# Kernel optimization log

Hardware: AMD Instinct MI355X
Metric: run time of the kernel (lower is better)

The kernel has to match this reference:

```python
import jax, jax.numpy as jnp
import numpy as np

USERNUM = 100_000
ITEMNUM = 50_000
EMBED_DIM = 64
N_INTERACTIONS = 2_000_000
NUM_LAYERS = 3
BATCH = 4096


def setup_inputs() -> dict:
    rng = np.random.default_rng(0)
    # random bipartite interactions: users 1..USERNUM, items 1..ITEMNUM
    u = rng.integers(1, USERNUM + 1, N_INTERACTIONS)
    it = rng.integers(1, ITEMNUM + 1, N_INTERACTIONS)
    # node ids: user k -> k, item j -> USERNUM + j (matches build_graph)
    rows = np.concatenate([u, USERNUM + it]).astype(np.int32)
    cols = np.concatenate([USERNUM + it, u]).astype(np.int32)
    n_nodes = USERNUM + ITEMNUM + 1
    # symmetric normalization D^-1/2 A D^-1/2 (duplicate edges sum, as in scipy COO)
    deg = np.bincount(rows, minlength=n_nodes).astype(np.float32)
    d_inv_sqrt = np.where(deg > 0, deg ** -0.5, 0.0).astype(np.float32)
    vals = (d_inv_sqrt[rows] * d_inv_sqrt[cols]).astype(np.float32)

    key = jax.random.key(0)
    k1, k2, k3, k4, k5 = jax.random.split(key, 5)
    # xavier_normal init: std = sqrt(2 / (fan_in + fan_out))
    u_std = np.sqrt(2.0 / (USERNUM + 1 + EMBED_DIM)).astype(np.float32)
    i_std = np.sqrt(2.0 / (ITEMNUM + 1 + EMBED_DIM)).astype(np.float32)
    user_table = jax.random.normal(k1, (USERNUM + 1, EMBED_DIM), jnp.float32) * u_std
    item_table = jax.random.normal(k2, (ITEMNUM + 1, EMBED_DIM), jnp.float32) * i_std

    user_ids = jax.random.randint(k3, (BATCH,), 0, USERNUM + 1)
    pos_seqs = jax.random.randint(k4, (BATCH,), 1, ITEMNUM + 1)
    neg_seqs = jax.random.randint(k5, (BATCH,), 1, ITEMNUM + 1)

    return {
        "user_table": user_table,
        "item_table": item_table,
        "vals": jnp.asarray(vals),
        "rows": jnp.asarray(rows),
        "cols": jnp.asarray(cols),
        "user_ids": user_ids,
        "pos_seqs": pos_seqs,
        "neg_seqs": neg_seqs,
    }


def reference(user_table, item_table, vals, rows, cols, user_ids, pos_seqs, neg_seqs):
    usernum = user_table.shape[0] - 1
    itemnum = item_table.shape[0] - 1
    n_nodes = usernum + itemnum + 1

    # ego embeddings: users 0..usernum, items 1..itemnum (skip item padding row)
    x = jnp.concatenate([user_table, item_table[1:]], axis=0)  # [n_nodes, D]

    # LightGCN propagation: x_{l+1} = A_norm @ x_l (SpMM via gather + segment_sum),
    # layer combination = mean over layers 0..NUM_LAYERS
    acc = x
    for _ in range(NUM_LAYERS):
        msgs = vals[:, None] * x[cols]              # [nnz, D]
        x = jax.ops.segment_sum(msgs, rows, num_segments=n_nodes)
        acc = acc + x
    all_emb = acc / (NUM_LAYERS + 1)

    uidx = jnp.clip(user_ids, 0, usernum)
    pidx = usernum + jnp.clip(pos_seqs, 1, itemnum)  # item j lives at row usernum + j
    nidx = usernum + jnp.clip(neg_seqs, 1, itemnum)

    u_emb = all_emb[uidx]
    pos_logits = jnp.sum(u_emb * all_emb[pidx], axis=-1)
    neg_logits = jnp.sum(u_emb * all_emb[nidx], axis=-1)
    return pos_logits, neg_logits
```

## Files before the change

### kernel.cpp

```cpp
#include <hip/hip_runtime.h>
#include <hip/hip_fp16.h>
#include <cstdint>
#include <cstddef>


typedef __attribute__((ext_vector_type(8))) _Float16 half8;

#define NB_SHIFT 8
#define BCAP 16000
#define P1_SRC 4096
#define P1_DIM 512

__global__ __launch_bounds__(P1_DIM) void partition_kernel(
    const int* __restrict__ rows, const int* __restrict__ cols,
    int* __restrict__ bucket_cursor, int* __restrict__ tmp,
    int M , int nb) {
    __shared__ int            lhist[1024];
    __shared__ int            loff[1024];
    __shared__ int            ldelta[1024];
    __shared__ int            wsum[8];
    __shared__ int            stage[2 * P1_SRC];
    __shared__ unsigned short bstage[2 * P1_SRC];
    int t = threadIdx.x;
    int lane = t & 63, wv = t >> 6;
    int base     = blockIdx.x * P1_SRC;
    int cnt_here = min(P1_SRC, M - base);
    int full4    = cnt_here >> 2;
    int rem      = cnt_here & 3;
    for (int i = t; i < 1024; i += P1_DIM) lhist[i] = 0;
    __syncthreads();
    const int4* rows4 = (const int4*)(rows + base);
    const int4* cols4 = (const int4*)(cols + base);
    int4 uu[2], vv[2];
    int  rka[8], rkb[8];
#pragma unroll
    for (int k = 0; k < 2; ++k) {
        int i4 = t + k * P1_DIM;
        if (i4 < full4) {
            uu[k] = rows4[i4];
            vv[k] = cols4[i4];
            int u4[4] = {uu[k].x, uu[k].y, uu[k].z, uu[k].w};
            int v4[4] = {vv[k].x, vv[k].y, vv[k].z, vv[k].w};
#pragma unroll
            for (int e = 0; e < 4; ++e) {
                rka[4 * k + e] = atomicAdd(&lhist[u4[e] >> NB_SHIFT], 1);
                rkb[4 * k + e] = atomicAdd(&lhist[v4[e] >> NB_SHIFT], 1);
            }
        }
    }
    int ur = 0, vr = 0, rkra = 0, rkrb = 0;
    bool has_rem = (t < rem);
    if (has_rem) {
        ur = rows[base + 4 * full4 + t];
        vr = cols[base + 4 * full4 + t];
        rkra = atomicAdd(&lhist[ur >> NB_SHIFT], 1);
        rkrb = atomicAdd(&lhist[vr >> NB_SHIFT], 1);
    }
    __syncthreads();
    int v0 = lhist[2 * t], v1 = lhist[2 * t + 1];
    int ts = v0 + v1;
    int sc = ts;
#pragma unroll
    for (int off = 1; off < 64; off <<= 1) {
        int x = __shfl_up(sc, off);
        if (lane >= off) sc += x;
    }
    if (lane == 63) wsum[wv] = sc;
    __syncthreads();
    int prefix = 0;
#pragma unroll
    for (int k = 0; k < 8; ++k) {
        int s = wsum[k];
        prefix += (k < wv) ? s : 0;
    }
    int run = prefix + sc - ts;
    loff[2 * t]     = run;
    loff[2 * t + 1] = run + v0;
#pragma unroll
    for (int k = 0; k < 2; ++k) {
        int b  = 2 * t + k;
        int vvk = (k == 0) ? v0 : v1;
        if (b < nb && vvk > 0) {
            int old = atomicAdd(&bucket_cursor[b], vvk);
            ldelta[b] = b * BCAP + old - loff[b];
        }
    }
    __syncthreads();
#pragma unroll
    for (int k = 0; k < 2; ++k) {
        int i4 = t + k * P1_DIM;
        if (i4 < full4) {
            int u4[4] = {uu[k].x, uu[k].y, uu[k].z, uu[k].w};
            int v4[4] = {vv[k].x, vv[k].y, vv[k].z, vv[k].w};
#pragma unroll
            for (int e = 0; e < 4; ++e) {
                int ub = u4[e] >> NB_SHIFT;
                int s1 = loff[ub] + rka[4 * k + e];
                stage[s1]  = ((u4[e] & 255) << 18) | v4[e];
                bstage[s1] = (unsigned short)ub;
                int vb = v4[e] >> NB_SHIFT;
                int s2 = loff[vb] + rkb[4 * k + e];
                stage[s2]  = ((v4[e] & 255) << 18) | u4[e];
                bstage[s2] = (unsigned short)vb;
            }
        }
    }
    if (has_rem) {
        int ub = ur >> NB_SHIFT;
        int s1 = loff[ub] + rkra;
        stage[s1]  = ((ur & 255) << 18) | vr;
        bstage[s1] = (unsigned short)ub;
        int vb = vr >> NB_SHIFT;
        int s2 = loff[vb] + rkrb;
        stage[s2]  = ((vr & 255) << 18) | ur;
        bstage[s2] = (unsigned short)vb;
    }
    __syncthreads();
    int total = 2 * cnt_here;
    for (int s = t; s < total; s += P1_DIM) {
        tmp[s + ldelta[bstage[s]]] = stage[s];
    }
}

__global__ __launch_bounds__(512) void finalize_kernel(
    const int* __restrict__ tmp, const int* __restrict__ bcur,
    int* __restrict__ row_ptr, float* __restrict__ dis,
    float* __restrict__ dis2, float* __restrict__ invd,
    int* __restrict__ cv, int n_nodes, int nb, int nnz) {
    __shared__ int rcnt[256];
    __shared__ int ccur[256];
    __shared__ int wsum[4];
    __shared__ int red[512];
    int b = blockIdx.x;
    int t = threadIdx.x;
    int lane = t & 63, wv = t >> 6;
    int partial = 0;
    for (int i = t; i < b; i += 512) partial += bcur[i];
    red[t] = partial;
    __syncthreads();
    for (int off = 256; off > 0; off >>= 1) {
        if (t < off) red[t] += red[t + off];
        __syncthreads();
    }
    int dbeg  = red[0];
    int count = bcur[b];
    int src   = b * BCAP;
    if (t < 256) rcnt[t] = 0;
    __syncthreads();
    for (int i = t; i < count; i += 512) {
        atomicAdd(&rcnt[tmp[src + i] >> 18], 1);
    }
    __syncthreads();
    int v = 0, sc = 0;
    if (t < 256) {
        v  = rcnt[t];
        sc = v;
#pragma unroll
        for (int off = 1; off < 64; off <<= 1) {
            int x = __shfl_up(sc, off);
            if (lane >= off) sc += x;
        }
        if (lane == 63) wsum[wv] = sc;
    }
    __syncthreads();
    if (t < 256) {
        int prefix = 0;
#pragma unroll
        for (int k = 0; k < 4; ++k) {
            int s = wsum[k];
            prefix += (k < wv) ? s : 0;
        }
        int ex = prefix + sc - v;
        ccur[t] = dbeg + ex;
        int row = (b << NB_SHIFT) + t;
        if (row < n_nodes) {
            row_ptr[row] = dbeg + ex;
            double dv = (double)v;
            dis[row]  = (v > 0) ? (float)(1.0 / sqrt(dv)) : 0.0f;
            dis2[row] = (v > 0) ? (float)(1.0 / dv) : 0.0f;
            invd[row] = (v > 0) ? (float)sqrt(dv) : 0.0f;
        }
    }
    if (b == nb - 1 && t == 0) row_ptr[n_nodes] = nnz;
    __syncthreads();
    for (int i = t; i < count; i += 512) {
        int p  = tmp[src + i];
        int rk = atomicAdd(&ccur[p >> 18], 1);
        cv[rk] = p & 0x3FFFF;
    }
}

__global__ __launch_bounds__(256) void convert_y0_kernel(
    const float4* __restrict__ ut4, const float4* __restrict__ it4,
    const float* __restrict__ dis, half8* __restrict__ Yh0,
    int usernum, int n_nodes) {
    int idx = blockIdx.x * 256 + threadIdx.x;
    int row = idx >> 3;
    if (row >= n_nodes) return;
    int c = idx & 7;
    float d = dis[row];
    const float4* srcp = (row <= usernum)
        ? (ut4 + (size_t)row * 16 + 2 * c)
        : (it4 + (size_t)(row - usernum) * 16 + 2 * c);
    float4 a = srcp[0];
    float4 e = srcp[1];
    half8 o;
    o[0] = (_Float16)(d * a.x); o[1] = (_Float16)(d * a.y);
    o[2] = (_Float16)(d * a.z); o[3] = (_Float16)(d * a.w);
    o[4] = (_Float16)(d * e.x); o[5] = (_Float16)(d * e.y);
    o[6] = (_Float16)(d * e.z); o[7] = (_Float16)(d * e.w);
    Yh0[(size_t)row * 8 + c] = o;
}

__device__ inline float csr_row_sum_h(const _Float16* __restrict__ Yh,
                                      const int* __restrict__ cv,
                                      int beg, int end, int g, int l8,
                                      float one) {
    float acc[8] = {0.f, 0.f, 0.f, 0.f, 0.f, 0.f, 0.f, 0.f};
    const char* Yb = (const char*)Yh;
    const char* cb = (const char*)cv;
    unsigned lo = (unsigned)l8 * 16u;
    int j = beg + g;
    for (; j + 8 < end; j += 16) {
        unsigned c0 = (unsigned)*(const int*)(cb + ((unsigned)j << 2));
        unsigned c1 = (unsigned)*(const int*)(cb + ((unsigned)(j + 8) << 2));
        half8 x0 = *(const half8*)(Yb + (c0 << 7) + lo);
        half8 x1 = *(const half8*)(Yb + (c1 << 7) + lo);
        half8 tt = x0 + x1;
#pragma unroll
        for (int k = 0; k < 8; ++k) {
            acc[k] += one * (float)tt[k];
        }
    }
    if (j < end) {
        unsigned c0 = (unsigned)*(const int*)(cb + ((unsigned)j << 2));
        half8 x0 = *(const half8*)(Yb + (c0 << 7) + lo);
#pragma unroll
        for (int k = 0; k < 8; ++k) {
            acc[k] += one * (float)x0[k];
        }
    }
    bool gb0 = (g & 1) != 0;
    bool gb1 = (g & 2) != 0;
    bool gb2 = (g & 4) != 0;
    float s0 = gb0 ? acc[0] : acc[4];
    float s1 = gb0 ? acc[1] : acc[5];
    float s2 = gb0 ? acc[2] : acc[6];
    float s3 = gb0 ? acc[3] : acc[7];
    float a0 = (gb0 ? acc[4] : acc[0]) + __shfl_xor(s0, 8);
    float a1 = (gb0 ? acc[5] : acc[1]) + __shfl_xor(s1, 8);
    float a2 = (gb0 ? acc[6] : acc[2]) + __shfl_xor(s2, 8);
    float a3 = (gb0 ? acc[7] : acc[3]) + __shfl_xor(s3, 8);
    float t0 = gb1 ? a0 : a2;
    float t1 = gb1 ? a1 : a3;
    float b0 = (gb1 ? a2 : a0) + __shfl_xor(t0, 16);
    float b1 = (gb1 ? a3 : a1) + __shfl_xor(t1, 16);
    float u = gb2 ? b0 : b1;
    float fin = (gb2 ? b1 : b0) + __shfl_xor(u, 32);
    return fin;
}

__device__ inline int lane_dim(int g, int l8) {
    return l8 * 8 + ((g & 1) * 4 + (g & 2) + (g >> 2));
}

__global__ __launch_bounds__(256) void spmm_y_kernel(
    const _Float16* __restrict__ Yin, _Float16* __restrict__ Yout,
    const int* __restrict__ row_ptr, const int* __restrict__ cv,
    const float* __restrict__ dis2, float one, int n_nodes) {
    int wid  = (blockIdx.x * blockDim.x + threadIdx.x) >> 6;
    int lane = threadIdx.x & 63;
    int g = lane >> 3, sub = lane & 7;
    int row = wid * 8 + g;
    bool ok = row < n_nodes;
    int beg = 0, end = 0;
    if (ok) {
        beg = row_ptr[row];
        end = row_ptr[row + 1];
    }
    float d2 = ok ? dis2[row] : 0.0f;
    const char* Yb = (const char*)Yin;
    const char* cb = (const char*)cv;
    unsigned lo = (unsigned)sub * 16u;
    float acc[8] = {0.f, 0.f, 0.f, 0.f, 0.f, 0.f, 0.f, 0.f};
    int len = end - beg;
    int mx = len;
    mx = max(mx, __shfl_xor(mx, 8));
    mx = max(mx, __shfl_xor(mx, 16));
    mx = max(mx, __shfl_xor(mx, 32));
    int iters = (mx + 7) >> 3;
    int j = beg;
    size_t jb = ((size_t)(unsigned)j) << 2;
    int r0 = *(const int*)(cb + jb);
    int r1 = *(const int*)(cb + jb + 4u);
    int r2 = *(const int*)(cb + jb + 8u);
    int r3 = *(const int*)(cb + jb + 12u);
    int r4 = *(const int*)(cb + jb + 16u);
    int r5 = *(const int*)(cb + jb + 20u);
    int r6 = *(const int*)(cb + jb + 24u);
    int r7 = *(const int*)(cb + jb + 28u);
    for (int it = 0; it < iters; ++it) {
        unsigned c0 = (unsigned)((j     < end) ? r0 : 0);
        unsigned c1 = (unsigned)((j + 1 < end) ? r1 : 0);
        unsigned c2 = (unsigned)((j + 2 < end) ? r2 : 0);
        unsigned c3 = (unsigned)((j + 3 < end) ? r3 : 0);
        unsigned c4 = (unsigned)((j + 4 < end) ? r4 : 0);
        unsigned c5 = (unsigned)((j + 5 < end) ? r5 : 0);
        unsigned c6 = (unsigned)((j + 6 < end) ? r6 : 0);
        unsigned c7 = (unsigned)((j + 7 < end) ? r7 : 0);
        half8 x0 = *(const half8*)(Yb + ((size_t)c0 << 7) + lo);
        half8 x1 = *(const half8*)(Yb + ((size_t)c1 << 7) + lo);
        half8 x2 = *(const half8*)(Yb + ((size_t)c2 << 7) + lo);
        half8 x3 = *(const half8*)(Yb + ((size_t)c3 << 7) + lo);
        half8 x4 = *(const half8*)(Yb + ((size_t)c4 << 7) + lo);
        half8 x5 = *(const half8*)(Yb + ((size_t)c5 << 7) + lo);
        half8 x6 = *(const half8*)(Yb + ((size_t)c6 << 7) + lo);
        half8 x7 = *(const half8*)(Yb + ((size_t)c7 << 7) + lo);
        j += 8;
        jb = ((size_t)(unsigned)j) << 2;
        r0 = *(const int*)(cb + jb);
        r1 = *(const int*)(cb + jb + 4u);
        r2 = *(const int*)(cb + jb + 8u);
        r3 = *(const int*)(cb + jb + 12u);
        r4 = *(const int*)(cb + jb + 16u);
        r5 = *(const int*)(cb + jb + 20u);
        r6 = *(const int*)(cb + jb + 24u);
        r7 = *(const int*)(cb + jb + 28u);
        half8 sA = (x0 + x1) + (x2 + x3);
        half8 sB = (x4 + x5) + (x6 + x7);
        half8 tt = sA + sB;
#pragma unroll
        for (int k = 0; k < 8; ++k) {
            acc[k] += one * (float)tt[k];
        }
    }
    if (ok) {
        half8 o;
#pragma unroll
        for (int k = 0; k < 8; ++k) o[k] = (_Float16)(acc[k] * d2);
        *(half8*)((char*)Yout + ((size_t)row << 7) + lo) = o;
    }
}

__global__ __launch_bounds__(256) void gather_logits_kernel(
    const float* __restrict__ ut, const float* __restrict__ itb,
    const _Float16* __restrict__ Y1, const _Float16* __restrict__ Y2,
    const int* __restrict__ row_ptr, const int* __restrict__ cv,
    const float* __restrict__ dis, const float* __restrict__ invd,
    const int* __restrict__ user_ids, const int* __restrict__ pos_seqs,
    const int* __restrict__ neg_seqs, float* __restrict__ out,
    float one, int usernum, int itemnum, int batch) {
    int w    = (blockIdx.x * blockDim.x + threadIdx.x) >> 6;
    int lane = threadIdx.x & 63;
    if (w >= batch) return;
    int g = lane >> 3, l8 = lane & 7;
    int d = lane_dim(g, l8);
    int idxs[3];
    int u = min(max(user_ids[w], 0), usernum);
    idxs[0] = u;
    int p = min(max(pos_seqs[w], 1), itemnum);
    idxs[1] = usernum + p;
    int nn = min(max(neg_seqs[w], 1), itemnum);
    idxs[2] = usernum + nn;
    float vals[3];
#pragma unroll
    for (int q = 0; q < 3; ++q) {
        int idx = idxs[q];
        int beg = row_ptr[idx];
        int end = row_ptr[idx + 1];
        float dr = dis[idx];
        float iv = invd[idx];
        float fin = csr_row_sum_h(Y2, cv, beg, end, g, l8, one);
        const float* base0 = (q == 0) ? (ut + (size_t)u * 64)
                                      : (itb + (size_t)(idx - usernum) * 64);
        float x0v = base0[d];
        float y1v = (float)Y1[(size_t)idx * 64 + d];
        float y2v = (float)Y2[(size_t)idx * 64 + d];
        vals[q] = x0v + iv * (y1v + y2v) + fin * dr;
    }
    float dp = vals[0] * vals[1];
    float dn = vals[0] * vals[2];
#pragma unroll
    for (int off = 1; off < 64; off <<= 1) {
        dp += __shfl_xor(dp, off);
        dn += __shfl_xor(dn, off);
    }
    if (lane == 0) {
        out[w]         = dp * 0.0625f;
        out[batch + w] = dn * 0.0625f;
    }
}

extern "C" void kernel_launch(void* const* d_in, const int* in_sizes, int n_in,
                              void* d_out, int out_size, void* d_ws,
                              size_t ws_size, hipStream_t stream) {
    const float* user_table = (const float*)d_in[0];
    const float* item_table = (const float*)d_in[1];
    const int*   rows       = (const int*)d_in[3];
    const int*   cols       = (const int*)d_in[4];
    const int*   user_ids   = (const int*)d_in[5];
    const int*   pos_seqs   = (const int*)d_in[6];
    const int*   neg_seqs   = (const int*)d_in[7];
    float*       out        = (float*)d_out;

    const int D = 64;
    int usernum = in_sizes[0] / D - 1;
    int itemnum = in_sizes[1] / D - 1;
    int nnz     = in_sizes[2];
    int batch   = in_sizes[5];
    int n_nodes = usernum + itemnum + 1;
    int nb      = (n_nodes + (1 << NB_SHIFT) - 1) >> NB_SHIFT;
    int M       = nnz >> 1;

    char* w = (char*)d_ws;
    auto alloc = [&](size_t bytes) {
        char* p = w;
        w += (bytes + 255) & ~(size_t)255;
        return p;
    };
    _Float16* Yh0   = (_Float16*)alloc((size_t)n_nodes * D * 2);
    _Float16* Yh1   = (_Float16*)alloc((size_t)n_nodes * D * 2);
    _Float16* Yh2   = (_Float16*)alloc((size_t)n_nodes * D * 2);
    int*   cv       = (int*)alloc((size_t)nnz * 4 + 8192);
    int*   row_ptr  = (int*)alloc((size_t)(n_nodes + 1) * 4);
    float* dis      = (float*)alloc((size_t)n_nodes * 4);
    float* dis2     = (float*)alloc((size_t)n_nodes * 4);
    float* invd     = (float*)alloc((size_t)n_nodes * 4);
    int*   bcur     = (int*)alloc(4096);
    int*   tmp      = (int*)Yh1;

    hipMemsetAsync(bcur, 0, 4096, stream);
    int p1_tiles = (M + P1_SRC - 1) / P1_SRC;
    partition_kernel<<<p1_tiles, P1_DIM, 0, stream>>>(rows, cols, bcur, tmp,
                                                      M, nb);
    finalize_kernel<<<nb, 512, 0, stream>>>(tmp, bcur, row_ptr, dis, dis2,
                                            invd, cv, n_nodes, nb, nnz);
    int conv_blocks = (n_nodes * 8 + 255) / 256;
    convert_y0_kernel<<<conv_blocks, 256, 0, stream>>>(
        (const float4*)user_table, (const float4*)item_table, dis,
        (half8*)Yh0, usernum, n_nodes);

    const float one = 1.0f;
    int spmm_grid = (n_nodes + 31) / 32;
    spmm_y_kernel<<<spmm_grid, 256, 0, stream>>>(Yh0, Yh1, row_ptr, cv, dis2,
                                                 one, n_nodes);
    spmm_y_kernel<<<spmm_grid, 256, 0, stream>>>(Yh1, Yh2, row_ptr, cv, dis2,
                                                 one, n_nodes);

    gather_logits_kernel<<<(batch + 3) / 4, 256, 0, stream>>>(
        user_table, item_table, Yh1, Yh2, row_ptr, cv, dis, invd, user_ids,
        pos_seqs, neg_seqs, out, one, usernum, itemnum, batch);
}
```

Measured before the change: 292.4 us.

## Split fp16 embeddings into two 32-dim halves processed by separate grid slices

Stores each layer's fp16 embedding matrix as two column halves (dims 0-31 and 32-63), each 64 bytes per row. The SpMM kernel gains a second grid dimension that selects the half and maps 4 lanes per row, so each wave handles 16 rows. The intent is to shrink the working set of each gather pass so it stays resident in cache, improving hit rates for the random column gathers. The cost is reading the CSR indices twice, once per half, plus more blocks and a slightly more complex gather in the logits kernel.

```diff
diff --git a/kernel.cpp b/kernel.cpp
--- a/kernel.cpp
+++ b/kernel.cpp
@@ -192,8 +192,8 @@
 
 __global__ __launch_bounds__(256) void convert_y0_kernel(
     const float4* __restrict__ ut4, const float4* __restrict__ it4,
-    const float* __restrict__ dis, half8* __restrict__ Yh0,
-    int usernum, int n_nodes) {
+    const float* __restrict__ dis, _Float16* __restrict__ YA,
+    _Float16* __restrict__ YB, int usernum, int n_nodes) {
     int idx = blockIdx.x * 256 + threadIdx.x;
     int row = idx >> 3;
     if (row >= n_nodes) return;
@@ -209,23 +209,26 @@
     o[2] = (_Float16)(d * a.z); o[3] = (_Float16)(d * a.w);
     o[4] = (_Float16)(d * e.x); o[5] = (_Float16)(d * e.y);
     o[6] = (_Float16)(d * e.z); o[7] = (_Float16)(d * e.w);
-    Yh0[(size_t)row * 8 + c] = o;
-}
-
-__device__ inline float csr_row_sum_h(const _Float16* __restrict__ Yh,
-                                      const int* __restrict__ cv,
-                                      int beg, int end, int g, int l8,
-                                      float one) {
+    _Float16* dst = (c < 4) ? (YA + (size_t)row * 32 + c * 8)
+                            : (YB + (size_t)row * 32 + (c - 4) * 8);
+    *(half8*)dst = o;
+}
+
+__device__ inline float csr_row_sum_h2(const _Float16* __restrict__ YA,
+                                       const _Float16* __restrict__ YB,
+                                       const int* __restrict__ cv,
+                                       int beg, int end, int g, int l8,
+                                       float one) {
     float acc[8] = {0.f, 0.f, 0.f, 0.f, 0.f, 0.f, 0.f, 0.f};
-    const char* Yb = (const char*)Yh;
+    const char* Yb = (const char*)(l8 < 4 ? YA : YB);
     const char* cb = (const char*)cv;
-    unsigned lo = (unsigned)l8 * 16u;
+    unsigned lo = (unsigned)(l8 & 3) * 16u;
     int j = beg + g;
     for (; j + 8 < end; j += 16) {
         unsigned c0 = (unsigned)*(const int*)(cb + ((unsigned)j << 2));
         unsigned c1 = (unsigned)*(const int*)(cb + ((unsigned)(j + 8) << 2));
-        half8 x0 = *(const half8*)(Yb + (c0 << 7) + lo);
-        half8 x1 = *(const half8*)(Yb + (c1 << 7) + lo);
+        half8 x0 = *(const half8*)(Yb + ((size_t)c0 << 6) + lo);
+        half8 x1 = *(const half8*)(Yb + ((size_t)c1 << 6) + lo);
         half8 tt = x0 + x1;
 #pragma unroll
         for (int k = 0; k < 8; ++k) {
@@ -234,7 +237,7 @@
     }
     if (j < end) {
         unsigned c0 = (unsigned)*(const int*)(cb + ((unsigned)j << 2));
-        half8 x0 = *(const half8*)(Yb + (c0 << 7) + lo);
+        half8 x0 = *(const half8*)(Yb + ((size_t)c0 << 6) + lo);
 #pragma unroll
         for (int k = 0; k < 8; ++k) {
             acc[k] += one * (float)x0[k];
@@ -265,13 +268,14 @@
 }
 
 __global__ __launch_bounds__(256) void spmm_y_kernel(
-    const _Float16* __restrict__ Yin, _Float16* __restrict__ Yout,
+    const _Float16* __restrict__ YinA, const _Float16* __restrict__ YinB,
+    _Float16* __restrict__ YoutA, _Float16* __restrict__ YoutB,
     const int* __restrict__ row_ptr, const int* __restrict__ cv,
     const float* __restrict__ dis2, float one, int n_nodes) {
     int wid  = (blockIdx.x * blockDim.x + threadIdx.x) >> 6;
     int lane = threadIdx.x & 63;
-    int g = lane >> 3, sub = lane & 7;
-    int row = wid * 8 + g;
+    int g = lane >> 2, sub = lane & 3;
+    int row = wid * 16 + g;
     bool ok = row < n_nodes;
     int beg = 0, end = 0;
     if (ok) {
@@ -279,12 +283,14 @@
         end = row_ptr[row + 1];
     }
     float d2 = ok ? dis2[row] : 0.0f;
-    const char* Yb = (const char*)Yin;
+    const char* Yb = (const char*)(blockIdx.y ? YinB : YinA);
+    _Float16*   Yo = blockIdx.y ? YoutB : YoutA;
     const char* cb = (const char*)cv;
     unsigned lo = (unsigned)sub * 16u;
     float acc[8] = {0.f, 0.f, 0.f, 0.f, 0.f, 0.f, 0.f, 0.f};
     int len = end - beg;
     int mx = len;
+    mx = max(mx, __shfl_xor(mx, 4));
     mx = max(mx, __shfl_xor(mx, 8));
     mx = max(mx, __shfl_xor(mx, 16));
     mx = max(mx, __shfl_xor(mx, 32));
@@ -308,14 +314,14 @@
         unsigned c5 = (unsigned)((j + 5 < end) ? r5 : 0);
         unsigned c6 = (unsigned)((j + 6 < end) ? r6 : 0);
         unsigned c7 = (unsigned)((j + 7 < end) ? r7 : 0);
-        half8 x0 = *(const half8*)(Yb + ((size_t)c0 << 7) + lo);
-        half8 x1 = *(const half8*)(Yb + ((size_t)c1 << 7) + lo);
-        half8 x2 = *(const half8*)(Yb + ((size_t)c2 << 7) + lo);
-        half8 x3 = *(const half8*)(Yb + ((size_t)c3 << 7) + lo);
-        half8 x4 = *(const half8*)(Yb + ((size_t)c4 << 7) + lo);
-        half8 x5 = *(const half8*)(Yb + ((size_t)c5 << 7) + lo);
-        half8 x6 = *(const half8*)(Yb + ((size_t)c6 << 7) + lo);
-        half8 x7 = *(const half8*)(Yb + ((size_t)c7 << 7) + lo);
+        half8 x0 = *(const half8*)(Yb + ((size_t)c0 << 6) + lo);
+        half8 x1 = *(const half8*)(Yb + ((size_t)c1 << 6) + lo);
+        half8 x2 = *(const half8*)(Yb + ((size_t)c2 << 6) + lo);
+        half8 x3 = *(const half8*)(Yb + ((size_t)c3 << 6) + lo);
+        half8 x4 = *(const half8*)(Yb + ((size_t)c4 << 6) + lo);
+        half8 x5 = *(const half8*)(Yb + ((size_t)c5 << 6) + lo);
+        half8 x6 = *(const half8*)(Yb + ((size_t)c6 << 6) + lo);
+        half8 x7 = *(const half8*)(Yb + ((size_t)c7 << 6) + lo);
         j += 8;
         jb = ((size_t)(unsigned)j) << 2;
         r0 = *(const int*)(cb + jb);
@@ -338,13 +344,14 @@
         half8 o;
 #pragma unroll
         for (int k = 0; k < 8; ++k) o[k] = (_Float16)(acc[k] * d2);
-        *(half8*)((char*)Yout + ((size_t)row << 7) + lo) = o;
+        *(half8*)((char*)Yo + (size_t)row * 64 + lo) = o;
     }
 }
 
 __global__ __launch_bounds__(256) void gather_logits_kernel(
     const float* __restrict__ ut, const float* __restrict__ itb,
-    const _Float16* __restrict__ Y1, const _Float16* __restrict__ Y2,
+    const _Float16* __restrict__ Y1A, const _Float16* __restrict__ Y1B,
+    const _Float16* __restrict__ Y2A, const _Float16* __restrict__ Y2B,
     const int* __restrict__ row_ptr, const int* __restrict__ cv,
     const float* __restrict__ dis, const float* __restrict__ invd,
     const int* __restrict__ user_ids, const int* __restrict__ pos_seqs,
@@ -370,12 +377,14 @@
         int end = row_ptr[idx + 1];
         float dr = dis[idx];
         float iv = invd[idx];
-        float fin = csr_row_sum_h(Y2, cv, beg, end, g, l8, one);
+        float fin = csr_row_sum_h2(Y2A, Y2B, cv, beg, end, g, l8, one);
         const float* base0 = (q == 0) ? (ut + (size_t)u * 64)
                                       : (itb + (size_t)(idx - usernum) * 64);
         float x0v = base0[d];
-        float y1v = (float)Y1[(size_t)idx * 64 + d];
-        float y2v = (float)Y2[(size_t)idx * 64 + d];
+        float y1v = (float)((d < 32) ? Y1A[(size_t)idx * 32 + d]
+                                     : Y1B[(size_t)idx * 32 + (d - 32)]);
+        float y2v = (float)((d < 32) ? Y2A[(size_t)idx * 32 + d]
+                                     : Y2B[(size_t)idx * 32 + (d - 32)]);
         vals[q] = x0v + iv * (y1v + y2v) + fin * dr;
     }
     float dp = vals[0] * vals[1];
@@ -418,16 +427,21 @@
         w += (bytes + 255) & ~(size_t)255;
         return p;
     };
-    _Float16* Yh0   = (_Float16*)alloc((size_t)n_nodes * D * 2);
-    _Float16* Yh1   = (_Float16*)alloc((size_t)n_nodes * D * 2);
-    _Float16* Yh2   = (_Float16*)alloc((size_t)n_nodes * D * 2);
+    size_t half_sz = (size_t)n_nodes * 32 * 2;
+    _Float16* YA0 = (_Float16*)alloc(half_sz);
+    _Float16* YB0 = (_Float16*)alloc(half_sz);
+    char* slab = alloc(4 * half_sz);
+    _Float16* YA1 = (_Float16*)(slab);
+    _Float16* YB1 = (_Float16*)(slab + half_sz);
+    _Float16* YA2 = (_Float16*)(slab + 2 * half_sz);
+    _Float16* YB2 = (_Float16*)(slab + 3 * half_sz);
     int*   cv       = (int*)alloc((size_t)nnz * 4 + 8192);
     int*   row_ptr  = (int*)alloc((size_t)(n_nodes + 1) * 4);
     float* dis      = (float*)alloc((size_t)n_nodes * 4);
     float* dis2     = (float*)alloc((size_t)n_nodes * 4);
     float* invd     = (float*)alloc((size_t)n_nodes * 4);
     int*   bcur     = (int*)alloc(4096);
-    int*   tmp      = (int*)Yh1;
+    int*   tmp      = (int*)slab;
 
     hipMemsetAsync(bcur, 0, 4096, stream);
     int p1_tiles = (M + P1_SRC - 1) / P1_SRC;
@@ -438,16 +452,16 @@
     int conv_blocks = (n_nodes * 8 + 255) / 256;
     convert_y0_kernel<<<conv_blocks, 256, 0, stream>>>(
         (const float4*)user_table, (const float4*)item_table, dis,
-        (half8*)Yh0, usernum, n_nodes);
+        YA0, YB0, usernum, n_nodes);
 
     const float one = 1.0f;
-    int spmm_grid = (n_nodes + 31) / 32;
-    spmm_y_kernel<<<spmm_grid, 256, 0, stream>>>(Yh0, Yh1, row_ptr, cv, dis2,
-                                                 one, n_nodes);
-    spmm_y_kernel<<<spmm_grid, 256, 0, stream>>>(Yh1, Yh2, row_ptr, cv, dis2,
-                                                 one, n_nodes);
+    dim3 spmm_grid((n_nodes + 63) / 64, 2);
+    spmm_y_kernel<<<spmm_grid, 256, 0, stream>>>(YA0, YB0, YA1, YB1, row_ptr,
+                                                 cv, dis2, one, n_nodes);
+    spmm_y_kernel<<<spmm_grid, 256, 0, stream>>>(YA1, YB1, YA2, YB2, row_ptr,
+                                                 cv, dis2, one, n_nodes);
 
     gather_logits_kernel<<<(batch + 3) / 4, 256, 0, stream>>>(
-        user_table, item_table, Yh1, Yh2, row_ptr, cv, dis, invd, user_ids,
-        pos_seqs, neg_seqs, out, one, usernum, itemnum, batch);
-}
+        user_table, item_table, YA1, YB1, YA2, YB2, row_ptr, cv, dis, invd,
+        user_ids, pos_seqs, neg_seqs, out, one, usernum, itemnum, batch);
+}
```

Measured after the change: 353.3 us. 20.8% more time.
